# Optimization experiments

Measured on AMD Instinct MI355X. Metric: run time of the kernel, lower is better.

The kernel has to match this reference:

```python
import jax, jax.numpy as jnp
import numpy as np

IMAGE_DIM = 224


def setup_inputs() -> dict:
    key = jax.random.key(0)
    k1, k2, k3, k4, k5 = jax.random.split(key, 5)
    N, H, W = 64, IMAGE_DIM, IMAGE_DIM
    im1 = jax.random.normal(k1, (N, 3, H, W), dtype=jnp.float32)
    im2 = jax.random.normal(k2, (N, 3, H, W), dtype=jnp.float32)
    C = jax.random.normal(k3, (N, 2, H, W), dtype=jnp.float32)
    M1 = jax.random.uniform(k4, (N, 1, H, W), dtype=jnp.float32)
    M2 = jax.random.uniform(k5, (N, 1, H, W), dtype=jnp.float32)
    return {"im1": im1, "im2": im2, "C": C, "M1": M1, "M2": M2}


def _grid(dtype):
    # q = [repeat(arange(H), W), tile(arange(W), H)], shape [2, H*W]
    x = jnp.repeat(jnp.arange(IMAGE_DIM), IMAGE_DIM)
    y = jnp.tile(jnp.arange(IMAGE_DIM), IMAGE_DIM)
    return jnp.stack([x, y]).astype(dtype)  # [2, HW]


def _bilinear_sample(imflat, qi):
    # imflat: [N, 3, HW], qi: [N, 2, HW] float coords
    HW = imflat.shape[-1]
    px, py = qi[:, 0], qi[:, 1]  # [N, HW]
    fx, cx = jnp.floor(px), jnp.ceil(px)
    fy, cy = jnp.floor(py), jnp.ceil(py)

    def gather_pixel(nx, ny):
        # weight = prod over axes of (1 - |point - neighbor|)
        w = (1.0 - jnp.abs(px - nx)) * (1.0 - jnp.abs(py - ny))  # [N, HW]
        ind = (nx + IMAGE_DIM * ny).astype(jnp.int32)
        ind = jnp.clip(ind, 0, HW - 1)  # guard against out-of-range neighbors
        pix = jnp.take_along_axis(imflat, ind[:, None, :], axis=2)  # [N, 3, HW]
        return w[:, None, :] * pix

    return (gather_pixel(fx, fy) + gather_pixel(cx, fy)
            + gather_pixel(fx, cy) + gather_pixel(cy * 0 + cx, cy))


def reference(im1, im2, C, M1, M2):
    N, ch, H, W = im1.shape
    HW = H * W
    q = _grid(im1.dtype)[None]              # [1, 2, HW]
    Cflat = C.reshape(N, 2, HW)
    a = _bilinear_sample(im1.reshape(N, ch, HW), q + Cflat).reshape(N, ch, H, W) * M1
    b = _bilinear_sample(im2.reshape(N, ch, HW), q - Cflat).reshape(N, ch, H, W) * M2
    return a + b
```

## Files before the change

kernel.cpp:

```cpp
#include <hip/hip_runtime.h>

#define IMG 224
#define HW (IMG * IMG)
#define TILE 32

__global__ __launch_bounds__(256, 5) void vm_kernel(
    const float* __restrict__ im1, const float* __restrict__ im2,
    const float* __restrict__ C, const float* __restrict__ M1,
    const float* __restrict__ M2, float* __restrict__ out)
{
    __shared__ float sC0[TILE][TILE + 1];
    __shared__ float sC1[TILE][TILE + 1];
    __shared__ float sM1[TILE][TILE + 1];
    __shared__ float sM2[TILE][TILE + 1];
    __shared__ float sO[3][TILE][TILE + 1];

    const int n    = blockIdx.y;
    const int tile = blockIdx.x;
    const int x0   = (tile / 7) * TILE;
    const int y0   = (tile % 7) * TILE;
    const int t    = threadIdx.x;

    const float* Cn  = C  + (size_t)n * 2 * HW;
    const float* M1n = M1 + (size_t)n * HW;
    const float* M2n = M2 + (size_t)n * HW;

#pragma unroll
    for (int j = 0; j < 4; ++j) {
        int idx = t + 256 * j;
        int tx  = idx >> 5;
        int ty  = idx & 31;
        int p   = (x0 + tx) * IMG + (y0 + ty);
        sC0[tx][ty] = Cn[p];
        sC1[tx][ty] = Cn[HW + p];
        sM1[tx][ty] = M1n[p];
        sM2[tx][ty] = M2n[p];
    }
    __syncthreads();

    const float* i1n = im1 + (size_t)n * 3 * HW;
    const float* i2n = im2 + (size_t)n * 3 * HW;

#pragma unroll
    for (int j = 0; j < 4; ++j) {
        int idx = t + 256 * j;
        int xl  = idx & 31;
        int yl  = idx >> 5;
        float c0 = sC0[xl][yl];
        float c1 = sC1[xl][yl];
        float m1 = sM1[xl][yl];
        float m2 = sM2[xl][yl];
        float xf = (float)(x0 + xl);
        float yf = (float)(y0 + yl);

        int   ia[4], ib[4];
        float wa[4], wb[4];

        {
            float px = xf + c0, py = yf + c1;
            float fx = floorf(px), cx = ceilf(px);
            float fy = floorf(py), cy = ceilf(py);
            float wfx = 1.0f - (px - fx), wcx = 1.0f - (cx - px);
            float wfy = 1.0f - (py - fy), wcy = 1.0f - (cy - py);
            ia[0] = min(max((int)fx + IMG * (int)fy, 0), HW - 1);
            ia[1] = min(max((int)cx + IMG * (int)fy, 0), HW - 1);
            ia[2] = min(max((int)fx + IMG * (int)cy, 0), HW - 1);
            ia[3] = min(max((int)cx + IMG * (int)cy, 0), HW - 1);
            wa[0] = wfx * wfy; wa[1] = wcx * wfy;
            wa[2] = wfx * wcy; wa[3] = wcx * wcy;
        }
        {
            float px = xf - c0, py = yf - c1;
            float fx = floorf(px), cx = ceilf(px);
            float fy = floorf(py), cy = ceilf(py);
            float wfx = 1.0f - (px - fx), wcx = 1.0f - (cx - px);
            float wfy = 1.0f - (py - fy), wcy = 1.0f - (cy - py);
            ib[0] = min(max((int)fx + IMG * (int)fy, 0), HW - 1);
            ib[1] = min(max((int)cx + IMG * (int)fy, 0), HW - 1);
            ib[2] = min(max((int)fx + IMG * (int)cy, 0), HW - 1);
            ib[3] = min(max((int)cx + IMG * (int)cy, 0), HW - 1);
            wb[0] = wfx * wfy; wb[1] = wcx * wfy;
            wb[2] = wfx * wcy; wb[3] = wcx * wcy;
        }

        float ra[12], rb[12];
#pragma unroll
        for (int ch = 0; ch < 3; ++ch) {
            const float* pa = i1n + ch * HW;
#pragma unroll
            for (int k = 0; k < 4; ++k) ra[ch * 4 + k] = pa[ia[k]];
        }
#pragma unroll
        for (int ch = 0; ch < 3; ++ch) {
            const float* pb = i2n + ch * HW;
#pragma unroll
            for (int k = 0; k < 4; ++k) rb[ch * 4 + k] = pb[ib[k]];
        }

#pragma unroll
        for (int ch = 0; ch < 3; ++ch) {
            float a = wa[0] * ra[ch * 4 + 0] + wa[1] * ra[ch * 4 + 1]
                    + wa[2] * ra[ch * 4 + 2] + wa[3] * ra[ch * 4 + 3];
            float b = wb[0] * rb[ch * 4 + 0] + wb[1] * rb[ch * 4 + 1]
                    + wb[2] * rb[ch * 4 + 2] + wb[3] * rb[ch * 4 + 3];
            sO[ch][xl][yl] = a * m1 + b * m2;
        }
    }
    __syncthreads();

    float* on = out + (size_t)n * 3 * HW;
#pragma unroll
    for (int j = 0; j < 4; ++j) {
        int idx = t + 256 * j;
        int tx  = idx >> 5;
        int ty  = idx & 31;
        int p   = (x0 + tx) * IMG + (y0 + ty);
#pragma unroll
        for (int ch = 0; ch < 3; ++ch) {
            on[ch * HW + p] = sO[ch][tx][ty];
        }
    }
}

extern "C" void kernel_launch(void* const* d_in, const int* in_sizes, int n_in,
                              void* d_out, int out_size, void* d_ws, size_t ws_size,
                              hipStream_t stream) {
    const float* im1 = (const float*)d_in[0];
    const float* im2 = (const float*)d_in[1];
    const float* C   = (const float*)d_in[2];
    const float* M1  = (const float*)d_in[3];
    const float* M2  = (const float*)d_in[4];
    float* out = (float*)d_out;
    dim3 grid(49, 64);
    vm_kernel<<<grid, 256, 0, stream>>>(im1, im2, C, M1, M2, out);
}
```

Measured before the change: 200.8 us.

## Stage padded image halo tiles in LDS for bilinear gathers with global fallback

Each block now loads a 42x42 padded region of each channel of im1 and im2 into shared memory, one channel at a time, and does the four-neighbour bilinear gathers from LDS. Whenever any lane in a wavefront has a neighbour outside the halo, the whole wavefront falls back to gathering from global memory. Coordinates, weights and offsets are computed once up front and kept in registers. The shared buffers are merged into one union array reused for the output tile. This is meant to replace scattered global gathers with coalesced tile loads, at the cost of more registers, extra barriers per channel, lower occupancy bounds, and the halo load going to waste when displacements exceed the pad (C is standard normal, so roughly 1.5% of offsets fall outside ±2.5).

```diff
diff --git a/kernel.cpp b/kernel.cpp
--- a/kernel.cpp
+++ b/kernel.cpp
@@ -3,23 +3,27 @@
 #define IMG 224
 #define HW (IMG * IMG)
 #define TILE 32
+#define PAD 5
+#define REG (TILE + 2 * PAD)
+#define RST (REG + 1)
+#define UT (TILE * (TILE + 1))
 
-__global__ __launch_bounds__(256, 5) void vm_kernel(
+__global__ __launch_bounds__(256, 4) void vm_kernel(
     const float* __restrict__ im1, const float* __restrict__ im2,
     const float* __restrict__ C, const float* __restrict__ M1,
     const float* __restrict__ M2, float* __restrict__ out)
 {
-    __shared__ float sC0[TILE][TILE + 1];
-    __shared__ float sC1[TILE][TILE + 1];
-    __shared__ float sM1[TILE][TILE + 1];
-    __shared__ float sM2[TILE][TILE + 1];
-    __shared__ float sO[3][TILE][TILE + 1];
+    __shared__ float uni[4 * UT];
+    __shared__ float sA[REG * RST];
+    __shared__ float sB[REG * RST];
 
     const int n    = blockIdx.y;
     const int tile = blockIdx.x;
     const int x0   = (tile / 7) * TILE;
     const int y0   = (tile % 7) * TILE;
     const int t    = threadIdx.x;
+    const int xlo  = x0 - PAD;
+    const int ylo  = y0 - PAD;
 
     const float* Cn  = C  + (size_t)n * 2 * HW;
     const float* M1n = M1 + (size_t)n * HW;
@@ -31,79 +35,123 @@
         int tx  = idx >> 5;
         int ty  = idx & 31;
         int p   = (x0 + tx) * IMG + (y0 + ty);
-        sC0[tx][ty] = Cn[p];
-        sC1[tx][ty] = Cn[HW + p];
-        sM1[tx][ty] = M1n[p];
-        sM2[tx][ty] = M2n[p];
+        uni[0 * UT + tx * 33 + ty] = Cn[p];
+        uni[1 * UT + tx * 33 + ty] = Cn[HW + p];
+        uni[2 * UT + tx * 33 + ty] = M1n[p];
+        uni[3 * UT + tx * 33 + ty] = M2n[p];
     }
     __syncthreads();
+    float c0[4], c1[4], m1v[4], m2v[4];
+#pragma unroll
+    for (int j = 0; j < 4; ++j) {
+        int idx = t + 256 * j;
+        int xl  = idx & 31;
+        int yl  = idx >> 5;
+        c0[j]  = uni[0 * UT + xl * 33 + yl];
+        c1[j]  = uni[1 * UT + xl * 33 + yl];
+        m1v[j] = uni[2 * UT + xl * 33 + yl];
+        m2v[j] = uni[3 * UT + xl * 33 + yl];
+    }
+    __syncthreads();
+
+    int   offA[4][4], offB[4][4];
+    float wA[4][4],   wB[4][4];
+    int   fa[4], fb[4];
+#pragma unroll
+    for (int j = 0; j < 4; ++j) {
+        int idx = t + 256 * j;
+        int xl  = idx & 31;
+        int yl  = idx >> 5;
+        float xf = (float)(x0 + xl);
+        float yf = (float)(y0 + yl);
+        {
+            float px = xf + c0[j], py = yf + c1[j];
+            float fx = floorf(px), cx = ceilf(px);
+            float fy = floorf(py), cy = ceilf(py);
+            float wfx = 1.0f - (px - fx), wcx = 1.0f - (cx - px);
+            float wfy = 1.0f - (py - fy), wcy = 1.0f - (cy - py);
+            wA[j][0] = wfx * wfy; wA[j][1] = wcx * wfy;
+            wA[j][2] = wfx * wcy; wA[j][3] = wcx * wcy;
+            int gx0 = (int)fx, gy0 = (int)fy;
+            int dx  = (int)cx - gx0, dy = (int)cy - gy0;
+            int q0  = gx0 - xlo, r0 = gy0 - ylo;
+            int o   = r0 * RST + q0;
+            offA[j][0] = o;            offA[j][1] = o + dx;
+            offA[j][2] = o + dy * RST; offA[j][3] = o + dx + dy * RST;
+            int f = (q0 >= 0) & (q0 + dx <= REG - 1) & (r0 >= 0) & (r0 + dy <= REG - 1);
+            fa[j] = __all(f);
+        }
+        {
+            float px = xf - c0[j], py = yf - c1[j];
+            float fx = floorf(px), cx = ceilf(px);
+            float fy = floorf(py), cy = ceilf(py);
+            float wfx = 1.0f - (px - fx), wcx = 1.0f - (cx - px);
+            float wfy = 1.0f - (py - fy), wcy = 1.0f - (cy - py);
+            wB[j][0] = wfx * wfy; wB[j][1] = wcx * wfy;
+            wB[j][2] = wfx * wcy; wB[j][3] = wcx * wcy;
+            int gx0 = (int)fx, gy0 = (int)fy;
+            int dx  = (int)cx - gx0, dy = (int)cy - gy0;
+            int q0  = gx0 - xlo, r0 = gy0 - ylo;
+            int o   = r0 * RST + q0;
+            offB[j][0] = o;            offB[j][1] = o + dx;
+            offB[j][2] = o + dy * RST; offB[j][3] = o + dx + dy * RST;
+            int f = (q0 >= 0) & (q0 + dx <= REG - 1) & (r0 >= 0) & (r0 + dy <= REG - 1);
+            fb[j] = __all(f);
+        }
+    }
 
     const float* i1n = im1 + (size_t)n * 3 * HW;
     const float* i2n = im2 + (size_t)n * 3 * HW;
 
 #pragma unroll
-    for (int j = 0; j < 4; ++j) {
-        int idx = t + 256 * j;
-        int xl  = idx & 31;
-        int yl  = idx >> 5;
-        float c0 = sC0[xl][yl];
-        float c1 = sC1[xl][yl];
-        float m1 = sM1[xl][yl];
-        float m2 = sM2[xl][yl];
-        float xf = (float)(x0 + xl);
-        float yf = (float)(y0 + yl);
-
-        int   ia[4], ib[4];
-        float wa[4], wb[4];
-
-        {
-            float px = xf + c0, py = yf + c1;
-            float fx = floorf(px), cx = ceilf(px);
-            float fy = floorf(py), cy = ceilf(py);
-            float wfx = 1.0f - (px - fx), wcx = 1.0f - (cx - px);
-            float wfy = 1.0f - (py - fy), wcy = 1.0f - (cy - py);
-            ia[0] = min(max((int)fx + IMG * (int)fy, 0), HW - 1);
-            ia[1] = min(max((int)cx + IMG * (int)fy, 0), HW - 1);
-            ia[2] = min(max((int)fx + IMG * (int)cy, 0), HW - 1);
-            ia[3] = min(max((int)cx + IMG * (int)cy, 0), HW - 1);
-            wa[0] = wfx * wfy; wa[1] = wcx * wfy;
-            wa[2] = wfx * wcy; wa[3] = wcx * wcy;
+    for (int ch = 0; ch < 3; ++ch) {
+        __syncthreads();
+        const float* pa = i1n + ch * HW;
+        const float* pb = i2n + ch * HW;
+        for (int e = t; e < REG * REG; e += 256) {
+            int r  = e / REG;
+            int c  = e - r * REG;
+            int gi = (xlo + c) + IMG * (ylo + r);
+            gi = min(max(gi, 0), HW - 1);
+            sA[r * RST + c] = pa[gi];
+            sB[r * RST + c] = pb[gi];
         }
-        {
-            float px = xf - c0, py = yf - c1;
-            float fx = floorf(px), cx = ceilf(px);
-            float fy = floorf(py), cy = ceilf(py);
-            float wfx = 1.0f - (px - fx), wcx = 1.0f - (cx - px);
-            float wfy = 1.0f - (py - fy), wcy = 1.0f - (cy - py);
-            ib[0] = min(max((int)fx + IMG * (int)fy, 0), HW - 1);
-            ib[1] = min(max((int)cx + IMG * (int)fy, 0), HW - 1);
-            ib[2] = min(max((int)fx + IMG * (int)cy, 0), HW - 1);
-            ib[3] = min(max((int)cx + IMG * (int)cy, 0), HW - 1);
-            wb[0] = wfx * wfy; wb[1] = wcx * wfy;
-            wb[2] = wfx * wcy; wb[3] = wcx * wcy;
-        }
-
-        float ra[12], rb[12];
+        __syncthreads();
 #pragma unroll
-        for (int ch = 0; ch < 3; ++ch) {
-            const float* pa = i1n + ch * HW;
-#pragma unroll
-            for (int k = 0; k < 4; ++k) ra[ch * 4 + k] = pa[ia[k]];
-        }
-#pragma unroll
-        for (int ch = 0; ch < 3; ++ch) {
-            const float* pb = i2n + ch * HW;
-#pragma unroll
-            for (int k = 0; k < 4; ++k) rb[ch * 4 + k] = pb[ib[k]];
-        }
-
-#pragma unroll
-        for (int ch = 0; ch < 3; ++ch) {
-            float a = wa[0] * ra[ch * 4 + 0] + wa[1] * ra[ch * 4 + 1]
-                    + wa[2] * ra[ch * 4 + 2] + wa[3] * ra[ch * 4 + 3];
-            float b = wb[0] * rb[ch * 4 + 0] + wb[1] * rb[ch * 4 + 1]
-                    + wb[2] * rb[ch * 4 + 2] + wb[3] * rb[ch * 4 + 3];
-            sO[ch][xl][yl] = a * m1 + b * m2;
+        for (int j = 0; j < 4; ++j) {
+            int idx = t + 256 * j;
+            int xl  = idx & 31;
+            int yl  = idx >> 5;
+            float a, b;
+            if (fa[j]) {
+                a = wA[j][0] * sA[offA[j][0]] + wA[j][1] * sA[offA[j][1]]
+                  + wA[j][2] * sA[offA[j][2]] + wA[j][3] * sA[offA[j][3]];
+            } else {
+                float px = (float)(x0 + xl) + c0[j], py = (float)(y0 + yl) + c1[j];
+                float fx = floorf(px), cx = ceilf(px);
+                float fy = floorf(py), cy = ceilf(py);
+                int i0 = min(max((int)fx + IMG * (int)fy, 0), HW - 1);
+                int i1 = min(max((int)cx + IMG * (int)fy, 0), HW - 1);
+                int i2 = min(max((int)fx + IMG * (int)cy, 0), HW - 1);
+                int i3 = min(max((int)cx + IMG * (int)cy, 0), HW - 1);
+                a = wA[j][0] * pa[i0] + wA[j][1] * pa[i1]
+                  + wA[j][2] * pa[i2] + wA[j][3] * pa[i3];
+            }
+            if (fb[j]) {
+                b = wB[j][0] * sB[offB[j][0]] + wB[j][1] * sB[offB[j][1]]
+                  + wB[j][2] * sB[offB[j][2]] + wB[j][3] * sB[offB[j][3]];
+            } else {
+                float px = (float)(x0 + xl) - c0[j], py = (float)(y0 + yl) - c1[j];
+                float fx = floorf(px), cx = ceilf(px);
+                float fy = floorf(py), cy = ceilf(py);
+                int i0 = min(max((int)fx + IMG * (int)fy, 0), HW - 1);
+                int i1 = min(max((int)cx + IMG * (int)fy, 0), HW - 1);
+                int i2 = min(max((int)fx + IMG * (int)cy, 0), HW - 1);
+                int i3 = min(max((int)cx + IMG * (int)cy, 0), HW - 1);
+                b = wB[j][0] * pb[i0] + wB[j][1] * pb[i1]
+                  + wB[j][2] * pb[i2] + wB[j][3] * pb[i3];
+            }
+            uni[ch * UT + xl * 33 + yl] = a * m1v[j] + b * m2v[j];
         }
     }
     __syncthreads();
@@ -117,7 +165,7 @@
         int p   = (x0 + tx) * IMG + (y0 + ty);
 #pragma unroll
         for (int ch = 0; ch < 3; ++ch) {
-            on[ch * HW + p] = sO[ch][tx][ty];
+            on[ch * HW + p] = uni[ch * UT + tx * 33 + ty];
         }
     }
 }
```

After: 196.6 us. -2.1%, faster.
